# Optimization experiments

Measured on AMD Instinct MI355X. Metric: run time of the kernel, lower is better.

## Reference

```python
import jax, jax.numpy as jnp
import numpy as np

THRESHOLD = 0.5

def _conv(x, w, b):
    y = jax.lax.conv_general_dilated(x, w, (1, 1), 'SAME',
                                     dimension_numbers=('NCHW', 'OIHW', 'NCHW'))
    return y + b[None, :, None, None]

def _gather2d(img, iy, ix):
    # img [B,C,H,W], iy/ix [B,h,w] int -> [B,C,h,w]
    return jax.vmap(lambda im, y, x: im[:, y, x])(img, iy, ix)

def _grid_sample_bilinear(img, grid):
    # torch F.grid_sample(mode='bilinear', padding_mode='border', align_corners=False)
    # img [B,C,H,W], grid [B,h,w,2] with (x,y) in [-1,1]
    B, C, H, W = img.shape
    x = (grid[..., 0] + 1.0) * (W * 0.5) - 0.5
    y = (grid[..., 1] + 1.0) * (H * 0.5) - 0.5
    x0 = jnp.floor(x); y0 = jnp.floor(y)
    wx = (x - x0)[:, None, :, :]; wy = (y - y0)[:, None, :, :]
    x0i = jnp.clip(x0.astype(jnp.int32), 0, W - 1)
    x1i = jnp.clip(x0.astype(jnp.int32) + 1, 0, W - 1)
    y0i = jnp.clip(y0.astype(jnp.int32), 0, H - 1)
    y1i = jnp.clip(y0.astype(jnp.int32) + 1, 0, H - 1)
    v00 = _gather2d(img, y0i, x0i); v01 = _gather2d(img, y0i, x1i)
    v10 = _gather2d(img, y1i, x0i); v11 = _gather2d(img, y1i, x1i)
    return (v00 * (1 - wx) * (1 - wy) + v01 * wx * (1 - wy)
            + v10 * (1 - wx) * wy + v11 * wx * wy)

def _encoder(lr, w_in, b_in, res_w, res_b):
    x = _conv(lr, w_in, b_in)
    for i in range(res_w.shape[0]):  # small fixed layer count
        r = _conv(jax.nn.relu(_conv(x, res_w[i, 0], res_b[i, 0])), res_w[i, 1], res_b[i, 1])
        x = x + r
    return x  # [B,64,Hl,Wl]

def _make_inp(feat, coord, cell):
    # nearest-sampled feature + relative coord + scaled cell (LIIF-style make_inp)
    B, C, Hl, Wl = feat.shape
    y = (coord[..., 0] + 1.0) * (Hl * 0.5) - 0.5
    x = (coord[..., 1] + 1.0) * (Wl * 0.5) - 0.5
    iyn = jnp.clip(jnp.floor(y + 0.5).astype(jnp.int32), 0, Hl - 1)
    ixn = jnp.clip(jnp.floor(x + 0.5).astype(jnp.int32), 0, Wl - 1)
    fs = _gather2d(feat, iyn, ixn).transpose(0, 2, 3, 1)  # [B,h,w,C]
    cy = (2.0 * iyn + 1.0) / Hl - 1.0
    cx = (2.0 * ixn + 1.0) / Wl - 1.0
    rel = jnp.stack([(coord[..., 0] - cy) * Hl, (coord[..., 1] - cx) * Wl], axis=-1)
    cell_s = cell * jnp.array([Hl, Wl], dtype=cell.dtype)
    return jnp.concatenate([fs, rel, cell_s], axis=-1)  # [B,h,w,C+4]

def setup_inputs() -> dict:
    key = jax.random.key(0)
    ks = jax.random.split(key, 16)
    B, Hl, Wl, h, w, C = 2, 96, 96, 384, 384, 64
    lr = jax.random.normal(ks[0], (B, 3, Hl, Wl), jnp.float32)
    ys = (jnp.arange(h, dtype=jnp.float32) + 0.5) / h * 2.0 - 1.0
    xs = (jnp.arange(w, dtype=jnp.float32) + 0.5) / w * 2.0 - 1.0
    gy, gx = jnp.meshgrid(ys, xs, indexing='ij')
    coord = jnp.broadcast_to(jnp.stack([gy, gx], -1), (B, h, w, 2))  # (y,x)
    cell = jnp.broadcast_to(jnp.array([2.0 / h, 2.0 / w], jnp.float32), (B, h, w, 2))
    def lin(k, fan_in, shape):
        return jax.random.normal(k, shape, jnp.float32) / np.sqrt(fan_in)
    D = C + 4  # 68
    return {
        'lr': lr, 'coord': coord, 'cell': cell,
        'enc_w_in': jax.random.normal(ks[1], (C, 3, 3, 3), jnp.float32) * 0.05,
        'enc_b_in': jnp.zeros((C,), jnp.float32),
        'enc_res_w': jax.random.normal(ks[2], (4, 2, C, C, 3, 3), jnp.float32) * 0.02,
        'enc_res_b': jnp.zeros((4, 2, C), jnp.float32),
        'cls_w1': lin(ks[3], D, (D, 64)), 'cls_b1': jnp.zeros((64,), jnp.float32),
        'cls_w2': lin(ks[4], 64, (64, 2)), 'cls_b2': jnp.zeros((2,), jnp.float32),
        'lw1': lin(ks[5], D, (D, 64)), 'lb1': jnp.zeros((64,), jnp.float32),
        'lw2': lin(ks[6], 64, (64, 64)), 'lb2': jnp.zeros((64,), jnp.float32),
        'lw3': lin(ks[7], 64, (64, 3)), 'lb3': jnp.zeros((3,), jnp.float32),
        'hw1': lin(ks[8], D, (D, 256)), 'hb1': jnp.zeros((256,), jnp.float32),
        'hmid_w': lin(ks[9], 256, (2, 256, 256)), 'hmid_b': jnp.zeros((2, 256), jnp.float32),
        'hw_out': lin(ks[10], 256, (256, 3)), 'hb_out': jnp.zeros((3,), jnp.float32),
    }

def reference(lr, coord, cell, enc_w_in, enc_b_in, enc_res_w, enc_res_b,
              cls_w1, cls_b1, cls_w2, cls_b2,
              lw1, lb1, lw2, lb2, lw3, lb3,
              hw1, hb1, hmid_w, hmid_b, hw_out, hb_out):
    feat = _encoder(lr, enc_w_in, enc_b_in, enc_res_w, enc_res_b)
    inp = _make_inp(feat, coord, cell)  # [B,h,w,68]
    # classifier -> softmax difficulty gate
    logits = jax.nn.relu(inp @ cls_w1 + cls_b1) @ cls_w2 + cls_b2
    diff = jax.nn.softmax(logits, axis=-1)
    hard = diff[..., 1] > THRESHOLD  # [B,h,w]
    # light sampler (dense over all pixels; where-select == gather/scatter dispatch)
    pl = jax.nn.relu(inp @ lw1 + lb1)
    pl = jax.nn.relu(pl @ lw2 + lb2)
    pl = pl @ lw3 + lb3
    # heavy sampler
    ph = jax.nn.relu(inp @ hw1 + hb1)
    for i in range(hmid_w.shape[0]):
        ph = jax.nn.relu(ph @ hmid_w[i] + hmid_b[i])
    ph = ph @ hw_out + hb_out
    pred = jnp.where(hard[..., None], ph, pl)  # [B,h,w,3]
    pred = pred.transpose(0, 3, 1, 2)  # [B,3,h,w]
    pred = pred + _grid_sample_bilinear(lr, coord[..., ::-1])  # coord.flip(-1) -> (x,y)
    ratio_easy = jnp.mean(1.0 - hard.astype(jnp.float32))
    return (pred, ratio_easy)
```

## Files before the change

kernel.cpp:

```cpp
#include <hip/hip_runtime.h>

#define HL 96
#define WL 96
#define HO 384
#define WO 384
#define NPIX (2*HO*WO)
#define FEAT_ELEMS ((size_t)2*64*HL*WL)
#define PLANE (HL*WL)
#define HGRID (NPIX/64)

typedef unsigned short us4 __attribute__((ext_vector_type(4)));
typedef unsigned short us8 __attribute__((ext_vector_type(8)));
typedef __bf16         b8  __attribute__((ext_vector_type(8)));
typedef float          f32x4 __attribute__((ext_vector_type(4)));

__device__ __forceinline__ unsigned short f2b(float x) {
  unsigned u = __builtin_bit_cast(unsigned, x);
  unsigned r = (u + 0x7FFFu + ((u >> 16) & 1u)) >> 16;
  return (unsigned short)r;
}

__device__ __forceinline__ f32x4 MF(us8 a, us8 b, f32x4 c) {
  return __builtin_amdgcn_mfma_f32_16x16x32_bf16(
      __builtin_bit_cast(b8, a), __builtin_bit_cast(b8, b), c, 0, 0, 0);
}

template<int CIN, int COPT, bool RELU, bool RES>
__global__ __launch_bounds__(256) void conv_s_k(
    const float* __restrict__ in, const float* __restrict__ wP,
    const float* __restrict__ bias, const float* __restrict__ res,
    float* __restrict__ out)
{
  const int t   = threadIdx.x;
  const int p   = blockIdx.x * 256 + t;
  const int co0 = blockIdx.y * COPT;
  const int b   = blockIdx.z;
  const int x   = p % WL;
  const bool xl = (x == 0), xr = (x == WL - 1);

  float acc[COPT];
  #pragma unroll
  for (int j = 0; j < COPT; ++j) acc[j] = bias[co0 + j];

  int  ic[3]; bool yv[3];
  int  im[3], ip[3];
  #pragma unroll
  for (int ky = 0; ky < 3; ++ky) {
    int pr = p + (ky - 1) * WL;
    yv[ky] = ((unsigned)pr < (unsigned)PLANE);
    ic[ky] = yv[ky] ? pr : 0;
    im[ky] = ic[ky] - 1; if (im[ky] < 0) im[ky] = 0;
    ip[ky] = ic[ky] + 1; if (ip[ky] > PLANE - 1) ip[ky] = PLANE - 1;
  }

  const float* inb = in + (size_t)b * CIN * PLANE;

  #pragma unroll 2
  for (int ci = 0; ci < CIN; ++ci) {
    const float* pl = inb + (size_t)ci * PLANE;
    #pragma unroll
    for (int ky = 0; ky < 3; ++ky) {
      float am = pl[im[ky]];
      float a0 = pl[ic[ky]];
      float ap = pl[ip[ky]];
      if (!yv[ky]) { am = 0.f; a0 = 0.f; ap = 0.f; }
      if (xl) am = 0.f;
      if (xr) ap = 0.f;
      const float* wrow = wP + (size_t)(ci * 9 + ky * 3) * 64 + co0;
      #pragma unroll
      for (int j = 0; j < COPT; ++j) acc[j] += am * wrow[j];
      #pragma unroll
      for (int j = 0; j < COPT; ++j) acc[j] += a0 * wrow[64 + j];
      #pragma unroll
      for (int j = 0; j < COPT; ++j) acc[j] += ap * wrow[128 + j];
    }
  }

  size_t ob = ((size_t)b * 64 + co0) * PLANE + p;
  #pragma unroll
  for (int j = 0; j < COPT; ++j) {
    float v = acc[j];
    if (RELU) v = fmaxf(v, 0.f);
    if (RES)  v += res[ob + (size_t)j * PLANE];
    out[ob + (size_t)j * PLANE] = v;
  }
}

template<bool RELU, bool RES>
__global__ __launch_bounds__(256) void conv_lw_k(
    const float* __restrict__ in, const float* __restrict__ wG,
    const float* __restrict__ bias, const float* __restrict__ res,
    float* __restrict__ out)
{
  __shared__ float sw[576 * 4];

  const int t   = threadIdx.x;
  const int p   = blockIdx.x * 256 + t;
  const int co0 = blockIdx.y * 4;
  const int b   = blockIdx.z;
  const int x   = p % WL;
  const bool xl = (x == 0), xr = (x == WL - 1);

  {
    const float4* s4 = (const float4*)(wG + (size_t)blockIdx.y * 2304);
    float4* d4 = (float4*)sw;
    for (int i = t; i < 576; i += 256) d4[i] = s4[i];
  }

  float acc[4];
  #pragma unroll
  for (int j = 0; j < 4; ++j) acc[j] = bias[co0 + j];

  int  ic[3]; bool yv[3];
  int  im[3], ip[3];
  #pragma unroll
  for (int ky = 0; ky < 3; ++ky) {
    int pr = p + (ky - 1) * WL;
    yv[ky] = ((unsigned)pr < (unsigned)PLANE);
    ic[ky] = yv[ky] ? pr : 0;
    im[ky] = ic[ky] - 1; if (im[ky] < 0) im[ky] = 0;
    ip[ky] = ic[ky] + 1; if (ip[ky] > PLANE - 1) ip[ky] = PLANE - 1;
  }

  const float* inb = in + (size_t)b * 64 * PLANE;
  __syncthreads();

  #pragma unroll 2
  for (int ci = 0; ci < 64; ++ci) {
    const float* pl = inb + (size_t)ci * PLANE;
    #pragma unroll
    for (int ky = 0; ky < 3; ++ky) {
      float am = pl[im[ky]];
      float a0 = pl[ic[ky]];
      float ap = pl[ip[ky]];
      if (!yv[ky]) { am = 0.f; a0 = 0.f; ap = 0.f; }
      if (xl) am = 0.f;
      if (xr) ap = 0.f;
      const float* wrow = &sw[(ci * 9 + ky * 3) * 4];
      #pragma unroll
      for (int j = 0; j < 4; ++j) acc[j] += am * wrow[j];
      #pragma unroll
      for (int j = 0; j < 4; ++j) acc[j] += a0 * wrow[4 + j];
      #pragma unroll
      for (int j = 0; j < 4; ++j) acc[j] += ap * wrow[8 + j];
    }
  }

  size_t ob = ((size_t)b * 64 + co0) * PLANE + p;
  #pragma unroll
  for (int j = 0; j < 4; ++j) {
    float v = acc[j];
    if (RELU) v = fmaxf(v, 0.f);
    if (RES)  v += res[ob + (size_t)j * PLANE];
    out[ob + (size_t)j * PLANE] = v;
  }
}

__device__ __forceinline__ void prep_bf16(const float* __restrict__ src,
    unsigned short* __restrict__ dst, int K, int N, int Kp, int i)
{
  int n = i / Kp, k = i - n * Kp;
  float v = (k < K && n < N) ? src[(size_t)k * N + n] : 0.f;
  dst[i] = f2b(v);
}
__device__ __forceinline__ void prep_conv(const float* __restrict__ src,
    float* __restrict__ dst, int cin, int i)
{
  int co = i % 64; int r = i / 64;
  int ci = r / 9, tap = r % 9;
  dst[i] = src[((size_t)co * cin + ci) * 9 + tap];
}
__device__ __forceinline__ void prep_conv2(const float* __restrict__ src,
    float* __restrict__ dst, int i)
{
  int j  = i & 3;
  int t2 = i >> 2;
  int cg = t2 / 576;
  int r  = t2 - cg * 576;
  int ci = r / 9, tap = r - ci * 9;
  int co = cg * 4 + j;
  dst[i] = src[((size_t)co * 64 + ci) * 9 + tap];
}

#define PREP_TOTAL 467648
__global__ __launch_bounds__(256) void prep_all_k(
    const float* __restrict__ lw1, const float* __restrict__ lw2,
    const float* __restrict__ lw3, const float* __restrict__ hw1,
    const float* __restrict__ hmw, const float* __restrict__ hwo,
    const float* __restrict__ enc_w_in, const float* __restrict__ enc_rw,
    unsigned short* __restrict__ lw1T, unsigned short* __restrict__ lw2T,
    unsigned short* __restrict__ lw3T, unsigned short* __restrict__ hw1T,
    unsigned short* __restrict__ hm0T, unsigned short* __restrict__ hm1T,
    unsigned short* __restrict__ hwoT, float* __restrict__ cwIn,
    float* __restrict__ cwRes)
{
  int i = blockIdx.x * 256 + threadIdx.x;
  if (i >= PREP_TOTAL) return;
  if (i < 6144)  { prep_bf16(lw1, lw1T, 68, 64, 96, i);    return; } i -= 6144;
  if (i < 4096)  { prep_bf16(lw2, lw2T, 64, 64, 64, i);    return; } i -= 4096;
  if (i < 1024)  { prep_bf16(lw3, lw3T, 64, 3, 64, i);     return; } i -= 1024;
  if (i < 24576) { prep_bf16(hw1, hw1T, 68, 256, 96, i);   return; } i -= 24576;
  if (i < 65536) { prep_bf16(hmw, hm0T, 256, 256, 256, i); return; } i -= 65536;
  if (i < 65536) { prep_bf16(hmw + 65536, hm1T, 256, 256, 256, i); return; } i -= 65536;
  if (i < 4096)  { prep_bf16(hwo, hwoT, 256, 3, 256, i);   return; } i -= 4096;
  if (i < 1728)  { prep_conv(enc_w_in, cwIn, 3, i);        return; } i -= 1728;
  int l = i / 36864, r = i % 36864;
  prep_conv2(enc_rw + (size_t)l * 36864, cwRes + (size_t)l * 36864, r);
}

__global__ __launch_bounds__(256) void nchw_to_nhwc_k(const float* __restrict__ in,
                                                      float* __restrict__ out)
{
  __shared__ float s[64][65];
  const int b = blockIdx.y;
  const int pix0 = blockIdx.x * 64;
  const int t = threadIdx.x;
  #pragma unroll
  for (int cc = 0; cc < 16; ++cc) {
    int co = cc * 4 + (t >> 6);
    int px = t & 63;
    s[px][co] = in[((size_t)b * 64 + co) * PLANE + pix0 + px];
  }
  __syncthreads();
  #pragma unroll
  for (int pp = 0; pp < 16; ++pp) {
    int px = pp * 4 + (t >> 6);
    int co = t & 63;
    out[((size_t)b * PLANE + pix0 + px) * 64 + co] = s[px][co];
  }
}

template<int NT, int KT>
__device__ __forceinline__ void mfma_compute(
    const unsigned short* __restrict__ aBase, int AS,
    const unsigned short* __restrict__ WT, int Kpad,
    int n0, int lane, f32x4 (&acc)[4][NT])
{
  const int lr = lane & 15;
  const int lc = lane >> 4;
  #pragma unroll
  for (int m = 0; m < 4; ++m)
    #pragma unroll
    for (int j = 0; j < NT; ++j) acc[m][j] = (f32x4){0.f, 0.f, 0.f, 0.f};

  const unsigned short* aP = aBase + lr * AS + lc * 8;
  const unsigned short* bP = WT + (size_t)(n0 + lr) * Kpad + lc * 8;

  constexpr int KCH = (KT >= 4) ? 4 : KT;
  #pragma unroll
  for (int kc = 0; kc < KT; kc += KCH) {
    us8 breg[KCH][NT];
    #pragma unroll
    for (int kk = 0; kk < KCH; ++kk)
      #pragma unroll
      for (int j = 0; j < NT; ++j)
        breg[kk][j] = *(const us8*)(bP + (size_t)j * 16 * Kpad + (kc + kk) * 32);
    #pragma unroll
    for (int kc2 = 0; kc2 < KCH; ++kc2) {
      us8 a0[4];
      #pragma unroll
      for (int m = 0; m < 4; ++m)
        a0[m] = *(const us8*)(aP + (m * 16) * AS + (kc + kc2) * 32);
      #pragma unroll
      for (int m = 0; m < 4; ++m)
        #pragma unroll
        for (int j = 0; j < NT; ++j)
          acc[m][j] = MF(a0[m], breg[kc2][j], acc[m][j]);
    }
  }
}

template<int NT, bool RELU>
__device__ __forceinline__ void mfma_store(
    const f32x4 (&acc)[4][NT], const float* __restrict__ bias,
    unsigned short* __restrict__ dBase, int DS, int dCol0, int n0, int lane)
{
  const int lr = lane & 15;
  const int lc = lane >> 4;
  #pragma unroll
  for (int j = 0; j < NT; ++j) {
    int n = n0 + j * 16 + lr;
    float bv = bias[n];
    #pragma unroll
    for (int m = 0; m < 4; ++m)
      #pragma unroll
      for (int r = 0; r < 4; ++r) {
        float v = acc[m][j][r] + bv;
        if (RELU) v = fmaxf(v, 0.f);
        dBase[(m * 16 + lc * 4 + r) * DS + dCol0 + n] = f2b(v);
      }
  }
}

template<int KT>
__device__ __forceinline__ void mfma_out3w(
    const unsigned short* __restrict__ aBase, int AS,
    const unsigned short* __restrict__ WT, int Kpad,
    const float* __restrict__ bias, float (*dst)[4], int mtile, int lane)
{
  const int lr = lane & 15;
  const int lc = lane >> 4;
  f32x4 acc = (f32x4){0.f, 0.f, 0.f, 0.f};
  const unsigned short* aP = aBase + (mtile * 16 + lr) * AS + lc * 8;
  const unsigned short* bP = WT + (size_t)lr * Kpad + lc * 8;

  constexpr int KCH = (KT >= 4) ? 4 : KT;
  #pragma unroll
  for (int kc = 0; kc < KT; kc += KCH) {
    us8 breg[KCH];
    #pragma unroll
    for (int kk = 0; kk < KCH; ++kk)
      breg[kk] = *(const us8*)(bP + (kc + kk) * 32);
    #pragma unroll
    for (int kk = 0; kk < KCH; ++kk) {
      us8 a = *(const us8*)(aP + (kc + kk) * 32);
      acc = MF(a, breg[kk], acc);
    }
  }
  if (lr < 3) {
    float bv = bias[lr];
    #pragma unroll
    for (int r = 0; r < 4; ++r)
      dst[mtile * 16 + lc * 4 + r][lr] = acc[r] + bv;
  }
}

__device__ __forceinline__ void nearest_idx(float gy, float gx, int& iy, int& ix)
{
  float fy = (gy + 1.f) * (HL * 0.5f) - 0.5f;
  float fx = (gx + 1.f) * (WL * 0.5f) - 0.5f;
  iy = min(max((int)floorf(fy + 0.5f), 0), HL - 1);
  ix = min(max((int)floorf(fx + 0.5f), 0), WL - 1);
}

__device__ __forceinline__ float bilinear_lr(const float* __restrict__ lrimg,
                                             int b, int ch, float gy, float gx)
{
  float x = (gx + 1.f) * (WL * 0.5f) - 0.5f;
  float y = (gy + 1.f) * (HL * 0.5f) - 0.5f;
  float xf = floorf(x), yf = floorf(y);
  float wx = x - xf, wy = y - yf;
  int x0i = min(max((int)xf,     0), WL - 1);
  int x1i = min(max((int)xf + 1, 0), WL - 1);
  int y0i = min(max((int)yf,     0), HL - 1);
  int y1i = min(max((int)yf + 1, 0), HL - 1);
  const float* img = lrimg + ((size_t)b * 3 + ch) * PLANE;
  float v00 = img[y0i * WL + x0i], v01 = img[y0i * WL + x1i];
  float v10 = img[y1i * WL + x0i], v11 = img[y1i * WL + x1i];
  return v00 * (1.f - wx) * (1.f - wy) + v01 * wx * (1.f - wy)
       + v10 * (1.f - wx) * wy + v11 * wx * wy;
}

template<int JB>
__device__ __forceinline__ void cls_block2(
    const float* __restrict__ fpA, const float* __restrict__ fpB,
    const float4& eA, const float4& eB,
    const float* __restrict__ cw1, const float* __restrict__ cb1,
    const float* __restrict__ cw2, int j0,
    float& l0a, float& l1a, float& l0b, float& l1b)
{
  float accA[JB], accB[JB];
  #pragma unroll
  for (int j = 0; j < JB; ++j) { accA[j] = cb1[j0 + j]; accB[j] = accA[j]; }
  #pragma unroll 4
  for (int kq = 0; kq < 16; ++kq) {
    float4 a4A = *(const float4*)(fpA + kq * 4);
    float4 a4B = *(const float4*)(fpB + kq * 4);
    float avA[4] = {a4A.x, a4A.y, a4A.z, a4A.w};
    float avB[4] = {a4B.x, a4B.y, a4B.z, a4B.w};
    #pragma unroll
    for (int kk = 0; kk < 4; ++kk) {
      const float* wr = cw1 + (size_t)(kq * 4 + kk) * 64 + j0;
      float aA = avA[kk], aB = avB[kk];
      #pragma unroll
      for (int j = 0; j < JB; ++j) { accA[j] += aA * wr[j]; accB[j] += aB * wr[j]; }
    }
  }
  {
    const float* wr = cw1 + (size_t)64 * 64 + j0;
    #pragma unroll
    for (int j = 0; j < JB; ++j) { accA[j] += eA.x * wr[j]; accB[j] += eB.x * wr[j]; }
    wr += 64;
    #pragma unroll
    for (int j = 0; j < JB; ++j) { accA[j] += eA.y * wr[j]; accB[j] += eB.y * wr[j]; }
    wr += 64;
    #pragma unroll
    for (int j = 0; j < JB; ++j) { accA[j] += eA.z * wr[j]; accB[j] += eB.z * wr[j]; }
    wr += 64;
    #pragma unroll
    for (int j = 0; j < JB; ++j) { accA[j] += eA.w * wr[j]; accB[j] += eB.w * wr[j]; }
  }
  #pragma unroll
  for (int j = 0; j < JB; ++j) {
    float hA = fmaxf(accA[j], 0.f);
    float hB = fmaxf(accB[j], 0.f);
    float w0 = cw2[(j0 + j) * 2 + 0], w1 = cw2[(j0 + j) * 2 + 1];
    l0a += hA * w0; l1a += hA * w1;
    l0b += hB * w0; l1b += hB * w1;
  }
}

__global__ __launch_bounds__(256, 4) void cls_gate2_k(
    const float* __restrict__ featT, const float* __restrict__ coord,
    const float* __restrict__ cell,
    const float* __restrict__ cw1, const float* __restrict__ cb1,
    const float* __restrict__ cw2, const float* __restrict__ cb2,
    int* __restrict__ counters, unsigned* __restrict__ easyList,
    unsigned* __restrict__ hardList)
{
  const int T  = blockIdx.x * 256 + threadIdx.x;
  const int gA = T * 2, gB = gA + 1;

  int bA = gA / (HO * WO);
  float gyA = coord[(size_t)gA * 2 + 0];
  float gxA = coord[(size_t)gA * 2 + 1];
  int iyA, ixA; nearest_idx(gyA, gxA, iyA, ixA);
  const float* fpA = featT + (((size_t)bA * PLANE) + iyA * WL + ixA) * 64;
  float4 eA;
  { float cy = (2.f * iyA + 1.f) / HL - 1.f;
    float cx = (2.f * ixA + 1.f) / WL - 1.f;
    eA.x = (gyA - cy) * HL; eA.y = (gxA - cx) * WL;
    eA.z = cell[(size_t)gA * 2 + 0] * HL; eA.w = cell[(size_t)gA * 2 + 1] * WL; }

  int bB = gB / (HO * WO);
  float gyB = coord[(size_t)gB * 2 + 0];
  float gxB = coord[(size_t)gB * 2 + 1];
  int iyB, ixB; nearest_idx(gyB, gxB, iyB, ixB);
  const float* fpB = featT + (((size_t)bB * PLANE) + iyB * WL + ixB) * 64;
  float4 eB;
  { float cy = (2.f * iyB + 1.f) / HL - 1.f;
    float cx = (2.f * ixB + 1.f) / WL - 1.f;
    eB.x = (gyB - cy) * HL; eB.y = (gxB - cx) * WL;
    eB.z = cell[(size_t)gB * 2 + 0] * HL; eB.w = cell[(size_t)gB * 2 + 1] * WL; }

  float l0a = cb2[0], l1a = cb2[1];
  float l0b = cb2[0], l1b = cb2[1];
  cls_block2<32>(fpA, fpB, eA, eB, cw1, cb1, cw2, 0,  l0a, l1a, l0b, l1b);
  cls_block2<32>(fpA, fpB, eA, eB, cw1, cb1, cw2, 32, l0a, l1a, l0b, l1b);
  bool hardA = (l1a > l0a);
  bool hardB = (l1b > l0b);

  unsigned long long mh0 = __ballot(hardA);
  unsigned long long mh1 = __ballot(hardB);
  int lane = threadIdx.x & 63;
  int nh0 = __popcll(mh0), nh1 = __popcll(mh1);
  int nh = nh0 + nh1;
  int baseH = 0, baseE = 0;
  if (lane == 0) {
    baseH = atomicAdd(&counters[1], nh);
    baseE = atomicAdd(&counters[0], 128 - nh);
  }
  baseH = __shfl(baseH, 0);
  baseE = __shfl(baseE, 0);
  unsigned long long below = (1ull << lane) - 1ull;
  int hbA = __popcll(mh0 & below);
  int hbB = nh0 + __popcll(mh1 & below);
  int ebA = lane - hbA;
  int ebB = (64 - nh0) + (lane - __popcll(mh1 & below));
  if (hardA) hardList[baseH + hbA] = (unsigned)gA;
  else       easyList[baseE + ebA] = (unsigned)gA;
  if (hardB) hardList[baseH + hbB] = (unsigned)gB;
  else       easyList[baseE + ebB] = (unsigned)gB;
}

__device__ __forceinline__ void build_inp_row(
    const float* __restrict__ featT, const float* __restrict__ coord,
    const float* __restrict__ cell, unsigned g, int p, int q8,
    unsigned short (*sInpB)[104])
{
  int b = g / (HO * WO);
  float gy = coord[(size_t)g * 2 + 0];
  float gx = coord[(size_t)g * 2 + 1];
  int iy, ix; nearest_idx(gy, gx, iy, ix);
  const float* fpt = featT + (((size_t)b * PLANE) + iy * WL + ix) * 64 + q8 * 8;
  float4 u0 = *(const float4*)fpt;
  float4 u1 = *(const float4*)(fpt + 4);
  us8 pk;
  pk[0]=f2b(u0.x); pk[1]=f2b(u0.y); pk[2]=f2b(u0.z); pk[3]=f2b(u0.w);
  pk[4]=f2b(u1.x); pk[5]=f2b(u1.y); pk[6]=f2b(u1.z); pk[7]=f2b(u1.w);
  *(us8*)&sInpB[p][q8 * 8] = pk;
  if (q8 == 0) {
    float cy = (2.f * iy + 1.f) / HL - 1.f;
    float cx = (2.f * ix + 1.f) / WL - 1.f;
    float e0 = (gy - cy) * HL, e1 = (gx - cx) * WL;
    float e2 = cell[(size_t)g * 2 + 0] * HL, e3 = cell[(size_t)g * 2 + 1] * WL;
    us4 pe; pe[0]=f2b(e0); pe[1]=f2b(e1); pe[2]=f2b(e2); pe[3]=f2b(e3);
    *(us4*)&sInpB[p][64] = pe;
  }
  if (q8 == 1) {
    us4 z = (us4){0,0,0,0};
    #pragma unroll
    for (int c = 0; c < 9; ++c) *(us4*)&sInpB[p][68 + c * 4] = z;
  }
}

__global__ __launch_bounds__(512, 4) void ml_k(
    const float* __restrict__ featT, const float* __restrict__ coord,
    const float* __restrict__ cell,  const float* __restrict__ lrimg,
    const float* __restrict__ lb1, const float* __restrict__ lb2,
    const float* __restrict__ lb3,
    const unsigned short* __restrict__ lw1T, const unsigned short* __restrict__ lw2T,
    const unsigned short* __restrict__ lw3T,
    const float* __restrict__ hb1, const float* __restrict__ hmb,
    const float* __restrict__ hbo,
    const unsigned short* __restrict__ hw1T, const unsigned short* __restrict__ hm0T,
    const unsigned short* __restrict__ hm1T, const unsigned short* __restrict__ hwoT,
    const int* __restrict__ counters,
    const unsigned* __restrict__ easyList, const unsigned* __restrict__ hardList,
    float* __restrict__ out)
{
  __shared__ unsigned short sBuf[64 * 264];
  __shared__ unsigned short sInpB[64][104];
  __shared__ float sP[64][4];
  __shared__ unsigned sIdx[64];

  const int t = threadIdx.x, lane = t & 63, w = t >> 6;
  const bool isH = (blockIdx.x < HGRID);

  if (isH) {
    const int nH = counters[1];
    const int g0 = blockIdx.x * 64;
    if (g0 >= nH) return;
    unsigned short (*sAct)[264] = (unsigned short (*)[264])sBuf;

    {
      const int p = t >> 3, q = t & 7;
      int i = g0 + p; if (i > nH - 1) i = nH - 1;
      unsigned g = hardList[i];
      if (q == 0) sIdx[p] = g;
      build_inp_row(featT, coord, cell, g, p, q, sInpB);
    }
    __syncthreads();

    { f32x4 acc[4][2];
      mfma_compute<2, 3>(&sInpB[0][0], 104, hw1T, 96, w * 32, lane, acc);
      mfma_store<2, true>(acc, hb1, &sAct[0][0], 264, 0, w * 32, lane); }
    __syncthreads();
    { f32x4 acc[4][2];
      mfma_compute<2, 8>(&sAct[0][0], 264, hm0T, 256, w * 32, lane, acc);
      __syncthreads();
      mfma_store<2, true>(acc, hmb, &sAct[0][0], 264, 0, w * 32, lane); }
    __syncthreads();
    { f32x4 acc[4][2];
      mfma_compute<2, 8>(&sAct[0][0], 264, hm1T, 256, w * 32, lane, acc);
      __syncthreads();
      mfma_store<2, true>(acc, hmb + 256, &sAct[0][0], 264, 0, w * 32, lane); }
    __syncthreads();
    if (w < 4) mfma_out3w<8>(&sAct[0][0], 264, hwoT, 256, hbo, sP, w, lane);
    __syncthreads();

    if (t < 192) {
      int p = t / 3, ch = t % 3;
      int i = g0 + p;
      if (i < nH) {
        unsigned g = sIdx[p];
        int b = g / (HO * WO);
        int rem = g % (HO * WO);
        int oy = rem / WO, ox = rem % WO;
        float gy = coord[(size_t)g * 2 + 0];
        float gx = coord[(size_t)g * 2 + 1];
        float v = bilinear_lr(lrimg, b, ch, gy, gx);
        out[(((size_t)b * 3 + ch) * HO + oy) * WO + ox] = sP[p][ch] + v;
      }
    }
  } else {
    const int nE = counters[0];
    const int g0 = (blockIdx.x - HGRID) * 64;
    if (g0 >= nE) return;
    unsigned short* sL1 = sBuf;
    unsigned short* sL2 = sBuf + 64 * 72;

    if (t < 256) {
      const int p = t >> 2, q = t & 3;
      int i = g0 + p; if (i > nE - 1) i = nE - 1;
      unsigned g = easyList[i];
      if (q == 0) sIdx[p] = g;
      build_inp_row(featT, coord, cell, g, p, q * 2,     sInpB);
      build_inp_row(featT, coord, cell, g, p, q * 2 + 1, sInpB);
    }
    __syncthreads();

    if (w < 4) {
      f32x4 acc[4][1];
      mfma_compute<1, 3>(&sInpB[0][0], 104, lw1T, 96, w * 16, lane, acc);
      mfma_store<1, true>(acc, lb1, sL1, 72, 0, w * 16, lane);
    }
    __syncthreads();
    if (w < 4) {
      f32x4 acc[4][1];
      mfma_compute<1, 2>(sL1, 72, lw2T, 64, w * 16, lane, acc);
      mfma_store<1, true>(acc, lb2, sL2, 72, 0, w * 16, lane);
    }
    __syncthreads();
    if (w < 4) mfma_out3w<2>(sL2, 72, lw3T, 64, lb3, sP, w, lane);
    __syncthreads();

    if (t < 192) {
      int p = t / 3, ch = t % 3;
      int i = g0 + p;
      if (i < nE) {
        unsigned g = sIdx[p];
        int b = g / (HO * WO);
        int rem = g % (HO * WO);
        int oy = rem / WO, ox = rem % WO;
        float gy = coord[(size_t)g * 2 + 0];
        float gx = coord[(size_t)g * 2 + 1];
        float v = bilinear_lr(lrimg, b, ch, gy, gx);
        out[(((size_t)b * 3 + ch) * HO + oy) * WO + ox] = sP[p][ch] + v;
      }
    }
  }
}

__global__ void finalize_k(const int* __restrict__ counters, float* __restrict__ out)
{
  out[(size_t)NPIX * 3] = (float)(counters[0]) / (float)NPIX;
}

extern "C" void kernel_launch(void* const* d_in, const int* in_sizes, int n_in,
                              void* d_out, int out_size, void* d_ws, size_t ws_size,
                              hipStream_t stream)
{
  const float* lr       = (const float*)d_in[0];
  const float* coord    = (const float*)d_in[1];
  const float* cell     = (const float*)d_in[2];
  const float* enc_w_in = (const float*)d_in[3];
  const float* enc_b_in = (const float*)d_in[4];
  const float* enc_rw   = (const float*)d_in[5];
  const float* enc_rb   = (const float*)d_in[6];
  const float* cw1      = (const float*)d_in[7];
  const float* cb1      = (const float*)d_in[8];
  const float* cw2      = (const float*)d_in[9];
  const float* cb2      = (const float*)d_in[10];
  const float* lw1      = (const float*)d_in[11];
  const float* lb1      = (const float*)d_in[12];
  const float* lw2      = (const float*)d_in[13];
  const float* lb2      = (const float*)d_in[14];
  const float* lw3      = (const float*)d_in[15];
  const float* lb3      = (const float*)d_in[16];
  const float* hw1      = (const float*)d_in[17];
  const float* hb1      = (const float*)d_in[18];
  const float* hmw      = (const float*)d_in[19];
  const float* hmb      = (const float*)d_in[20];
  const float* hwo      = (const float*)d_in[21];
  const float* hbo      = (const float*)d_in[22];
  float* out = (float*)d_out;

  char* ws = (char*)d_ws;
  float* xA    = (float*)(ws + 1024);
  float* tmp   = xA  + FEAT_ELEMS;
  float* xB    = tmp + FEAT_ELEMS;
  float* featT = tmp;
  unsigned short* wb = (unsigned short*)(xB + FEAT_ELEMS);
  unsigned short* lw1T = wb;
  unsigned short* lw2T = lw1T + 64*96;
  unsigned short* lw3T = lw2T + 64*64;
  unsigned short* hw1T = lw3T + 16*64;
  unsigned short* hm0T = hw1T + 256*96;
  unsigned short* hm1T = hm0T + 65536;
  unsigned short* hwoT = hm1T + 65536;
  const size_t nb16 = 64*96 + 64*64 + 16*64 + 256*96 + 2*65536 + 16*256;
  float* cwIn  = (float*)(wb + nb16);
  float* cwRes = cwIn + 1728;
  size_t need = 1024 + 3 * FEAT_ELEMS * sizeof(float)
              + nb16 * 2 + (1728 + 8 * 36864) * sizeof(float);
  if (ws_size < need) return;

  int*      counters = (int*)xB;
  unsigned* easyList = (unsigned*)(xB + 16);
  unsigned* hardList = easyList + NPIX;

  prep_all_k<<<(PREP_TOTAL + 255) / 256, 256, 0, stream>>>(
      lw1, lw2, lw3, hw1, hmw, hwo, enc_w_in, enc_rw,
      lw1T, lw2T, lw3T, hw1T, hm0T, hm1T, hwoT, cwIn, cwRes);

  dim3 cgrid(36, 16, 2);
  conv_s_k<3, 4, false, false><<<cgrid, 256, 0, stream>>>(lr, cwIn, enc_b_in, nullptr, xA);

  float* cur = xA; float* oth = xB;
  for (int i = 0; i < 4; ++i) {
    const float* wp0 = cwRes + (size_t)(2 * i)     * 36864;
    const float* wp1 = cwRes + (size_t)(2 * i + 1) * 36864;
    const float* b0 = enc_rb + i * 128;
    const float* b1 = b0 + 64;
    conv_lw_k<true,  false><<<cgrid, 256, 0, stream>>>(cur, wp0, b0, nullptr, tmp);
    conv_lw_k<false, true ><<<cgrid, 256, 0, stream>>>(tmp, wp1, b1, cur, oth);
    float* sw2 = cur; cur = oth; oth = sw2;
  }

  nchw_to_nhwc_k<<<dim3(144, 2), 256, 0, stream>>>(cur, featT);

  hipMemsetAsync(counters, 0, 16, stream);

  cls_gate2_k<<<NPIX / 512, 256, 0, stream>>>(featT, coord, cell,
      cw1, cb1, cw2, cb2, counters, easyList, hardList);

  ml_k<<<2 * HGRID, 512, 0, stream>>>(featT, coord, cell, lr,
      lb1, lb2, lb3, lw1T, lw2T, lw3T,
      hb1, hmb, hbo, hw1T, hm0T, hm1T, hwoT,
      counters, easyList, hardList, out);

  finalize_k<<<1, 1, 0, stream>>>(counters, out);
}
```

Before: 604.9 us.

## Register-tile residual convs over 4 horizontal pixels with float4 loads

New measurement: 1.033 ms. +70.8%, slower.

```diff
diff --git a/kernel.cpp b/kernel.cpp
--- a/kernel.cpp
+++ b/kernel.cpp
@@ -86,73 +86,71 @@
   }
 }
 
-template<bool RELU, bool RES>
-__global__ __launch_bounds__(256) void conv_lw_k(
-    const float* __restrict__ in, const float* __restrict__ wG,
+template<int COPT, bool RELU, bool RES>
+__global__ __launch_bounds__(256) void conv4x_k(
+    const float* __restrict__ in, const float* __restrict__ wP,
     const float* __restrict__ bias, const float* __restrict__ res,
     float* __restrict__ out)
 {
-  __shared__ float sw[576 * 4];
-
-  const int t   = threadIdx.x;
-  const int p   = blockIdx.x * 256 + t;
-  const int co0 = blockIdx.y * 4;
-  const int b   = blockIdx.z;
-  const int x   = p % WL;
-  const bool xl = (x == 0), xr = (x == WL - 1);
-
-  {
-    const float4* s4 = (const float4*)(wG + (size_t)blockIdx.y * 2304);
-    float4* d4 = (float4*)sw;
-    for (int i = t; i < 576; i += 256) d4[i] = s4[i];
-  }
-
-  float acc[4];
-  #pragma unroll
-  for (int j = 0; j < 4; ++j) acc[j] = bias[co0 + j];
-
-  int  ic[3]; bool yv[3];
-  int  im[3], ip[3];
-  #pragma unroll
-  for (int ky = 0; ky < 3; ++ky) {
-    int pr = p + (ky - 1) * WL;
-    yv[ky] = ((unsigned)pr < (unsigned)PLANE);
-    ic[ky] = yv[ky] ? pr : 0;
-    im[ky] = ic[ky] - 1; if (im[ky] < 0) im[ky] = 0;
-    ip[ky] = ic[ky] + 1; if (ip[ky] > PLANE - 1) ip[ky] = PLANE - 1;
+  const int t    = threadIdx.x;
+  const int quad = blockIdx.x * 256 + t;
+  const int y    = quad / 24;
+  const int x0   = (quad % 24) * 4;
+  const int co0  = blockIdx.y * COPT;
+  const int b    = blockIdx.z;
+  const bool xL  = (x0 == 0);
+  const bool xR  = (x0 == WL - 4);
+
+  float acc[4][COPT];
+  #pragma unroll
+  for (int p = 0; p < 4; ++p)
+    #pragma unroll
+    for (int j = 0; j < COPT; ++j) acc[p][j] = bias[co0 + j];
+
+  int  rowOff[3]; bool rv[3];
+  #pragma unroll
+  for (int rr = 0; rr < 3; ++rr) {
+    int ry = y - 1 + rr;
+    rv[rr] = (ry >= 0 && ry < HL);
+    rowOff[rr] = (rv[rr] ? ry : 0) * WL;
   }
 
   const float* inb = in + (size_t)b * 64 * PLANE;
-  __syncthreads();
-
-  #pragma unroll 2
+
   for (int ci = 0; ci < 64; ++ci) {
     const float* pl = inb + (size_t)ci * PLANE;
     #pragma unroll
     for (int ky = 0; ky < 3; ++ky) {
-      float am = pl[im[ky]];
-      float a0 = pl[ic[ky]];
-      float ap = pl[ip[ky]];
-      if (!yv[ky]) { am = 0.f; a0 = 0.f; ap = 0.f; }
-      if (xl) am = 0.f;
-      if (xr) ap = 0.f;
-      const float* wrow = &sw[(ci * 9 + ky * 3) * 4];
-      #pragma unroll
-      for (int j = 0; j < 4; ++j) acc[j] += am * wrow[j];
-      #pragma unroll
-      for (int j = 0; j < 4; ++j) acc[j] += a0 * wrow[4 + j];
-      #pragma unroll
-      for (int j = 0; j < 4; ++j) acc[j] += ap * wrow[8 + j];
-    }
-  }
-
-  size_t ob = ((size_t)b * 64 + co0) * PLANE + p;
-  #pragma unroll
-  for (int j = 0; j < 4; ++j) {
-    float v = acc[j];
-    if (RELU) v = fmaxf(v, 0.f);
-    if (RES)  v += res[ob + (size_t)j * PLANE];
-    out[ob + (size_t)j * PLANE] = v;
+      const float* row = pl + rowOff[ky];
+      float4 m = *(const float4*)(row + x0);
+      float vL = xL ? 0.f : row[x0 - 1];
+      float vR = xR ? 0.f : row[x0 + 4];
+      if (!rv[ky]) { m.x = 0.f; m.y = 0.f; m.z = 0.f; m.w = 0.f; vL = 0.f; vR = 0.f; }
+      const float* wrow = wP + (size_t)(ci * 9 + ky * 3) * 64 + co0;
+      #pragma unroll
+      for (int j = 0; j < COPT; ++j) {
+        float w0 = wrow[j], w1 = wrow[64 + j], w2 = wrow[128 + j];
+        acc[0][j] += vL  * w0; acc[0][j] += m.x * w1; acc[0][j] += m.y * w2;
+        acc[1][j] += m.x * w0; acc[1][j] += m.y * w1; acc[1][j] += m.z * w2;
+        acc[2][j] += m.y * w0; acc[2][j] += m.z * w1; acc[2][j] += m.w * w2;
+        acc[3][j] += m.z * w0; acc[3][j] += m.w * w1; acc[3][j] += vR  * w2;
+      }
+    }
+  }
+
+  size_t ob = ((size_t)b * 64 + co0) * PLANE + y * WL + x0;
+  #pragma unroll
+  for (int j = 0; j < COPT; ++j) {
+    float4 v; v.x = acc[0][j]; v.y = acc[1][j]; v.z = acc[2][j]; v.w = acc[3][j];
+    if (RELU) {
+      v.x = fmaxf(v.x, 0.f); v.y = fmaxf(v.y, 0.f);
+      v.z = fmaxf(v.z, 0.f); v.w = fmaxf(v.w, 0.f);
+    }
+    if (RES) {
+      float4 r = *(const float4*)(res + ob + (size_t)j * PLANE);
+      v.x += r.x; v.y += r.y; v.z += r.z; v.w += r.w;
+    }
+    *(float4*)(out + ob + (size_t)j * PLANE) = v;
   }
 }
 
@@ -169,17 +167,6 @@
   int co = i % 64; int r = i / 64;
   int ci = r / 9, tap = r % 9;
   dst[i] = src[((size_t)co * cin + ci) * 9 + tap];
-}
-__device__ __forceinline__ void prep_conv2(const float* __restrict__ src,
-    float* __restrict__ dst, int i)
-{
-  int j  = i & 3;
-  int t2 = i >> 2;
-  int cg = t2 / 576;
-  int r  = t2 - cg * 576;
-  int ci = r / 9, tap = r - ci * 9;
-  int co = cg * 4 + j;
-  dst[i] = src[((size_t)co * 64 + ci) * 9 + tap];
 }
 
 #define PREP_TOTAL 467648
@@ -205,7 +192,7 @@
   if (i < 4096)  { prep_bf16(hwo, hwoT, 256, 3, 256, i);   return; } i -= 4096;
   if (i < 1728)  { prep_conv(enc_w_in, cwIn, 3, i);        return; } i -= 1728;
   int l = i / 36864, r = i % 36864;
-  prep_conv2(enc_rw + (size_t)l * 36864, cwRes + (size_t)l * 36864, r);
+  prep_conv(enc_rw + (size_t)l * 36864, cwRes + (size_t)l * 36864, 64, r);
 }
 
 __global__ __launch_bounds__(256) void nchw_to_nhwc_k(const float* __restrict__ in,
@@ -674,8 +661,9 @@
       lw1, lw2, lw3, hw1, hmw, hwo, enc_w_in, enc_rw,
       lw1T, lw2T, lw3T, hw1T, hm0T, hm1T, hwoT, cwIn, cwRes);
 
-  dim3 cgrid(36, 16, 2);
-  conv_s_k<3, 4, false, false><<<cgrid, 256, 0, stream>>>(lr, cwIn, enc_b_in, nullptr, xA);
+  dim3 cgrid1(36, 16, 2);
+  dim3 cgrid4(9, 32, 2);
+  conv_s_k<3, 4, false, false><<<cgrid1, 256, 0, stream>>>(lr, cwIn, enc_b_in, nullptr, xA);
 
   float* cur = xA; float* oth = xB;
   for (int i = 0; i < 4; ++i) {
@@ -683,8 +671,8 @@
     const float* wp1 = cwRes + (size_t)(2 * i + 1) * 36864;
     const float* b0 = enc_rb + i * 128;
     const float* b1 = b0 + 64;
-    conv_lw_k<true,  false><<<cgrid, 256, 0, stream>>>(cur, wp0, b0, nullptr, tmp);
-    conv_lw_k<false, true ><<<cgrid, 256, 0, stream>>>(tmp, wp1, b1, cur, oth);
+    conv4x_k<2, true,  false><<<cgrid4, 256, 0, stream>>>(cur, wp0, b0, nullptr, tmp);
+    conv4x_k<2, false, true ><<<cgrid4, 256, 0, stream>>>(tmp, wp1, b1, cur, oth);
     float* sw2 = cur; cur = oth; oth = sw2;
   }
 
```

## Split fused MLP kernel into heavy and light kernels with 128-row heavy tiles

Applied to the files above, without the earlier changes.

New measurement: 606.5 us. No clear change (+0.3%).

```diff
diff --git a/kernel.cpp b/kernel.cpp
--- a/kernel.cpp
+++ b/kernel.cpp
@@ -7,7 +7,6 @@
 #define NPIX (2*HO*WO)
 #define FEAT_ELEMS ((size_t)2*64*HL*WL)
 #define PLANE (HL*WL)
-#define HGRID (NPIX/64)
 
 typedef unsigned short us4 __attribute__((ext_vector_type(4)));
 typedef unsigned short us8 __attribute__((ext_vector_type(8)));
@@ -230,16 +229,16 @@
   }
 }
 
-template<int NT, int KT>
+template<int NT, int KT, int MT>
 __device__ __forceinline__ void mfma_compute(
     const unsigned short* __restrict__ aBase, int AS,
     const unsigned short* __restrict__ WT, int Kpad,
-    int n0, int lane, f32x4 (&acc)[4][NT])
+    int n0, int lane, f32x4 (&acc)[MT][NT])
 {
   const int lr = lane & 15;
   const int lc = lane >> 4;
   #pragma unroll
-  for (int m = 0; m < 4; ++m)
+  for (int m = 0; m < MT; ++m)
     #pragma unroll
     for (int j = 0; j < NT; ++j) acc[m][j] = (f32x4){0.f, 0.f, 0.f, 0.f};
 
@@ -257,12 +256,12 @@
         breg[kk][j] = *(const us8*)(bP + (size_t)j * 16 * Kpad + (kc + kk) * 32);
     #pragma unroll
     for (int kc2 = 0; kc2 < KCH; ++kc2) {
-      us8 a0[4];
-      #pragma unroll
-      for (int m = 0; m < 4; ++m)
+      us8 a0[MT];
+      #pragma unroll
+      for (int m = 0; m < MT; ++m)
         a0[m] = *(const us8*)(aP + (m * 16) * AS + (kc + kc2) * 32);
       #pragma unroll
-      for (int m = 0; m < 4; ++m)
+      for (int m = 0; m < MT; ++m)
         #pragma unroll
         for (int j = 0; j < NT; ++j)
           acc[m][j] = MF(a0[m], breg[kc2][j], acc[m][j]);
@@ -270,9 +269,9 @@
   }
 }
 
-template<int NT, bool RELU>
+template<int NT, bool RELU, int MT>
 __device__ __forceinline__ void mfma_store(
-    const f32x4 (&acc)[4][NT], const float* __restrict__ bias,
+    const f32x4 (&acc)[MT][NT], const float* __restrict__ bias,
     unsigned short* __restrict__ dBase, int DS, int dCol0, int n0, int lane)
 {
   const int lr = lane & 15;
@@ -282,7 +281,7 @@
     int n = n0 + j * 16 + lr;
     float bv = bias[n];
     #pragma unroll
-    for (int m = 0; m < 4; ++m)
+    for (int m = 0; m < MT; ++m)
       #pragma unroll
       for (int r = 0; r < 4; ++r) {
         float v = acc[m][j][r] + bv;
@@ -466,7 +465,7 @@
 __device__ __forceinline__ void build_inp_row(
     const float* __restrict__ featT, const float* __restrict__ coord,
     const float* __restrict__ cell, unsigned g, int p, int q8,
-    unsigned short (*sInpB)[104])
+    unsigned short* __restrict__ sInpB)
 {
   int b = g / (HO * WO);
   float gy = coord[(size_t)g * 2 + 0];
@@ -478,136 +477,144 @@
   us8 pk;
   pk[0]=f2b(u0.x); pk[1]=f2b(u0.y); pk[2]=f2b(u0.z); pk[3]=f2b(u0.w);
   pk[4]=f2b(u1.x); pk[5]=f2b(u1.y); pk[6]=f2b(u1.z); pk[7]=f2b(u1.w);
-  *(us8*)&sInpB[p][q8 * 8] = pk;
+  *(us8*)&sInpB[p * 104 + q8 * 8] = pk;
   if (q8 == 0) {
     float cy = (2.f * iy + 1.f) / HL - 1.f;
     float cx = (2.f * ix + 1.f) / WL - 1.f;
     float e0 = (gy - cy) * HL, e1 = (gx - cx) * WL;
     float e2 = cell[(size_t)g * 2 + 0] * HL, e3 = cell[(size_t)g * 2 + 1] * WL;
     us4 pe; pe[0]=f2b(e0); pe[1]=f2b(e1); pe[2]=f2b(e2); pe[3]=f2b(e3);
-    *(us4*)&sInpB[p][64] = pe;
+    *(us4*)&sInpB[p * 104 + 64] = pe;
   }
   if (q8 == 1) {
     us4 z = (us4){0,0,0,0};
     #pragma unroll
-    for (int c = 0; c < 9; ++c) *(us4*)&sInpB[p][68 + c * 4] = z;
-  }
-}
-
-__global__ __launch_bounds__(512, 4) void ml_k(
+    for (int c = 0; c < 9; ++c) *(us4*)&sInpB[p * 104 + 68 + c * 4] = z;
+  }
+}
+
+#define HLDS (128*104*2 + 128*264*2 + 128*4*4 + 128*4)
+
+__global__ __launch_bounds__(512, 2) void heavy_k(
+    const float* __restrict__ featT, const float* __restrict__ coord,
+    const float* __restrict__ cell,  const float* __restrict__ lrimg,
+    const float* __restrict__ hb1, const float* __restrict__ hmb,
+    const float* __restrict__ hbo,
+    const unsigned short* __restrict__ hw1T, const unsigned short* __restrict__ hm0T,
+    const unsigned short* __restrict__ hm1T, const unsigned short* __restrict__ hwoT,
+    const int* __restrict__ counters, const unsigned* __restrict__ list,
+    float* __restrict__ out)
+{
+  extern __shared__ char smem[];
+  unsigned short* sInpB = (unsigned short*)smem;
+  unsigned short* sAct  = (unsigned short*)(smem + 128*104*2);
+  float (*sP)[4]        = (float (*)[4])(smem + 128*104*2 + 128*264*2);
+  unsigned* sIdx        = (unsigned*)(smem + 128*104*2 + 128*264*2 + 128*16);
+
+  const int nH = counters[1];
+  const int g0 = blockIdx.x * 128;
+  if (g0 >= nH) return;
+
+  const int t = threadIdx.x, lane = t & 63, w = t >> 6;
+
+  {
+    const int p = t >> 2, q = t & 3;
+    int i = g0 + p; if (i > nH - 1) i = nH - 1;
+    unsigned g = list[i];
+    if (q == 0) sIdx[p] = g;
+    build_inp_row(featT, coord, cell, g, p, q * 2,     sInpB);
+    build_inp_row(featT, coord, cell, g, p, q * 2 + 1, sInpB);
+  }
+  __syncthreads();
+
+  { f32x4 acc[8][2];
+    mfma_compute<2, 3, 8>(sInpB, 104, hw1T, 96, w * 32, lane, acc);
+    mfma_store<2, true, 8>(acc, hb1, sAct, 264, 0, w * 32, lane); }
+  __syncthreads();
+  { f32x4 acc[8][2];
+    mfma_compute<2, 8, 8>(sAct, 264, hm0T, 256, w * 32, lane, acc);
+    __syncthreads();
+    mfma_store<2, true, 8>(acc, hmb, sAct, 264, 0, w * 32, lane); }
+  __syncthreads();
+  { f32x4 acc[8][2];
+    mfma_compute<2, 8, 8>(sAct, 264, hm1T, 256, w * 32, lane, acc);
+    __syncthreads();
+    mfma_store<2, true, 8>(acc, hmb + 256, sAct, 264, 0, w * 32, lane); }
+  __syncthreads();
+  mfma_out3w<8>(sAct, 264, hwoT, 256, hbo, sP, w, lane);
+  __syncthreads();
+
+  if (t < 384) {
+    int p = t / 3, ch = t % 3;
+    int i = g0 + p;
+    if (i < nH) {
+      unsigned g = sIdx[p];
+      int b = g / (HO * WO);
+      int rem = g % (HO * WO);
+      int oy = rem / WO, ox = rem % WO;
+      float gy = coord[(size_t)g * 2 + 0];
+      float gx = coord[(size_t)g * 2 + 1];
+      float v = bilinear_lr(lrimg, b, ch, gy, gx);
+      out[(((size_t)b * 3 + ch) * HO + oy) * WO + ox] = sP[p][ch] + v;
+    }
+  }
+}
+
+__global__ __launch_bounds__(256, 4) void light_k(
     const float* __restrict__ featT, const float* __restrict__ coord,
     const float* __restrict__ cell,  const float* __restrict__ lrimg,
     const float* __restrict__ lb1, const float* __restrict__ lb2,
     const float* __restrict__ lb3,
     const unsigned short* __restrict__ lw1T, const unsigned short* __restrict__ lw2T,
     const unsigned short* __restrict__ lw3T,
-    const float* __restrict__ hb1, const float* __restrict__ hmb,
-    const float* __restrict__ hbo,
-    const unsigned short* __restrict__ hw1T, const unsigned short* __restrict__ hm0T,
-    const unsigned short* __restrict__ hm1T, const unsigned short* __restrict__ hwoT,
-    const int* __restrict__ counters,
-    const unsigned* __restrict__ easyList, const unsigned* __restrict__ hardList,
+    const int* __restrict__ counters, const unsigned* __restrict__ list,
     float* __restrict__ out)
 {
-  __shared__ unsigned short sBuf[64 * 264];
-  __shared__ unsigned short sInpB[64][104];
+  const int nE = counters[0];
+  const int g0 = blockIdx.x * 64;
+  if (g0 >= nE) return;
+
+  __shared__ unsigned short sInpB[64 * 104];
+  __shared__ unsigned short sL1[64 * 72];
+  __shared__ unsigned short sL2[64 * 72];
   __shared__ float sP[64][4];
   __shared__ unsigned sIdx[64];
 
   const int t = threadIdx.x, lane = t & 63, w = t >> 6;
-  const bool isH = (blockIdx.x < HGRID);
-
-  if (isH) {
-    const int nH = counters[1];
-    const int g0 = blockIdx.x * 64;
-    if (g0 >= nH) return;
-    unsigned short (*sAct)[264] = (unsigned short (*)[264])sBuf;
-
-    {
-      const int p = t >> 3, q = t & 7;
-      int i = g0 + p; if (i > nH - 1) i = nH - 1;
-      unsigned g = hardList[i];
-      if (q == 0) sIdx[p] = g;
-      build_inp_row(featT, coord, cell, g, p, q, sInpB);
-    }
-    __syncthreads();
-
-    { f32x4 acc[4][2];
-      mfma_compute<2, 3>(&sInpB[0][0], 104, hw1T, 96, w * 32, lane, acc);
-      mfma_store<2, true>(acc, hb1, &sAct[0][0], 264, 0, w * 32, lane); }
-    __syncthreads();
-    { f32x4 acc[4][2];
-      mfma_compute<2, 8>(&sAct[0][0], 264, hm0T, 256, w * 32, lane, acc);
-      __syncthreads();
-      mfma_store<2, true>(acc, hmb, &sAct[0][0], 264, 0, w * 32, lane); }
-    __syncthreads();
-    { f32x4 acc[4][2];
-      mfma_compute<2, 8>(&sAct[0][0], 264, hm1T, 256, w * 32, lane, acc);
-      __syncthreads();
-      mfma_store<2, true>(acc, hmb + 256, &sAct[0][0], 264, 0, w * 32, lane); }
-    __syncthreads();
-    if (w < 4) mfma_out3w<8>(&sAct[0][0], 264, hwoT, 256, hbo, sP, w, lane);
-    __syncthreads();
-
-    if (t < 192) {
-      int p = t / 3, ch = t % 3;
-      int i = g0 + p;
-      if (i < nH) {
-        unsigned g = sIdx[p];
-        int b = g / (HO * WO);
-        int rem = g % (HO * WO);
-        int oy = rem / WO, ox = rem % WO;
-        float gy = coord[(size_t)g * 2 + 0];
-        float gx = coord[(size_t)g * 2 + 1];
-        float v = bilinear_lr(lrimg, b, ch, gy, gx);
-        out[(((size_t)b * 3 + ch) * HO + oy) * WO + ox] = sP[p][ch] + v;
-      }
-    }
-  } else {
-    const int nE = counters[0];
-    const int g0 = (blockIdx.x - HGRID) * 64;
-    if (g0 >= nE) return;
-    unsigned short* sL1 = sBuf;
-    unsigned short* sL2 = sBuf + 64 * 72;
-
-    if (t < 256) {
-      const int p = t >> 2, q = t & 3;
-      int i = g0 + p; if (i > nE - 1) i = nE - 1;
-      unsigned g = easyList[i];
-      if (q == 0) sIdx[p] = g;
-      build_inp_row(featT, coord, cell, g, p, q * 2,     sInpB);
-      build_inp_row(featT, coord, cell, g, p, q * 2 + 1, sInpB);
-    }
-    __syncthreads();
-
-    if (w < 4) {
-      f32x4 acc[4][1];
-      mfma_compute<1, 3>(&sInpB[0][0], 104, lw1T, 96, w * 16, lane, acc);
-      mfma_store<1, true>(acc, lb1, sL1, 72, 0, w * 16, lane);
-    }
-    __syncthreads();
-    if (w < 4) {
-      f32x4 acc[4][1];
-      mfma_compute<1, 2>(sL1, 72, lw2T, 64, w * 16, lane, acc);
-      mfma_store<1, true>(acc, lb2, sL2, 72, 0, w * 16, lane);
-    }
-    __syncthreads();
-    if (w < 4) mfma_out3w<2>(sL2, 72, lw3T, 64, lb3, sP, w, lane);
-    __syncthreads();
-
-    if (t < 192) {
-      int p = t / 3, ch = t % 3;
-      int i = g0 + p;
-      if (i < nE) {
-        unsigned g = sIdx[p];
-        int b = g / (HO * WO);
-        int rem = g % (HO * WO);
-        int oy = rem / WO, ox = rem % WO;
-        float gy = coord[(size_t)g * 2 + 0];
-        float gx = coord[(size_t)g * 2 + 1];
-        float v = bilinear_lr(lrimg, b, ch, gy, gx);
-        out[(((size_t)b * 3 + ch) * HO + oy) * WO + ox] = sP[p][ch] + v;
-      }
+
+  {
+    const int p = t >> 2, q = t & 3;
+    int i = g0 + p; if (i > nE - 1) i = nE - 1;
+    unsigned g = list[i];
+    if (q == 0) sIdx[p] = g;
+    build_inp_row(featT, coord, cell, g, p, q * 2,     sInpB);
+    build_inp_row(featT, coord, cell, g, p, q * 2 + 1, sInpB);
+  }
+  __syncthreads();
+
+  { f32x4 acc[4][1];
+    mfma_compute<1, 3, 4>(sInpB, 104, lw1T, 96, w * 16, lane, acc);
+    mfma_store<1, true, 4>(acc, lb1, sL1, 72, 0, w * 16, lane); }
+  __syncthreads();
+  { f32x4 acc[4][1];
+    mfma_compute<1, 2, 4>(sL1, 72, lw2T, 64, w * 16, lane, acc);
+    mfma_store<1, true, 4>(acc, lb2, sL2, 72, 0, w * 16, lane); }
+  __syncthreads();
+  mfma_out3w<2>(sL2, 72, lw3T, 64, lb3, sP, w, lane);
+  __syncthreads();
+
+  if (t < 192) {
+    int p = t / 3, ch = t % 3;
+    int i = g0 + p;
+    if (i < nE) {
+      unsigned g = sIdx[p];
+      int b = g / (HO * WO);
+      int rem = g % (HO * WO);
+      int oy = rem / WO, ox = rem % WO;
+      float gy = coord[(size_t)g * 2 + 0];
+      float gx = coord[(size_t)g * 2 + 1];
+      float v = bilinear_lr(lrimg, b, ch, gy, gx);
+      out[(((size_t)b * 3 + ch) * HO + oy) * WO + ox] = sP[p][ch] + v;
     }
   }
 }
@@ -670,6 +677,9 @@
   unsigned* easyList = (unsigned*)(xB + 16);
   unsigned* hardList = easyList + NPIX;
 
+  hipFuncSetAttribute((const void*)heavy_k,
+                      hipFuncAttributeMaxDynamicSharedMemorySize, HLDS);
+
   prep_all_k<<<(PREP_TOTAL + 255) / 256, 256, 0, stream>>>(
       lw1, lw2, lw3, hw1, hmw, hwo, enc_w_in, enc_rw,
       lw1T, lw2T, lw3T, hw1T, hm0T, hm1T, hwoT, cwIn, cwRes);
@@ -695,10 +705,11 @@
   cls_gate2_k<<<NPIX / 512, 256, 0, stream>>>(featT, coord, cell,
       cw1, cb1, cw2, cb2, counters, easyList, hardList);
 
-  ml_k<<<2 * HGRID, 512, 0, stream>>>(featT, coord, cell, lr,
-      lb1, lb2, lb3, lw1T, lw2T, lw3T,
-      hb1, hmb, hbo, hw1T, hm0T, hm1T, hwoT,
-      counters, easyList, hardList, out);
+  heavy_k<<<NPIX / 128, 512, HLDS, stream>>>(featT, coord, cell, lr,
+      hb1, hmb, hbo, hw1T, hm0T, hm1T, hwoT, counters, hardList, out);
+
+  light_k<<<NPIX / 64, 256, 0, stream>>>(featT, coord, cell, lr,
+      lb1, lb2, lb3, lw1T, lw2T, lw3T, counters, easyList, out);
 
   finalize_k<<<1, 1, 0, stream>>>(counters, out);
 }
```
